# Kernel tuning notes

Measured on AMD Instinct MI355X. Metric: run time of the kernel, lower is better.

Reference implementation:

```python
import jax, jax.numpy as jnp
import numpy as np

EMBED = 1024
HEADS = 16
HEAD_DIM = EMBED // HEADS


def setup_inputs() -> dict:
    key = jax.random.key(0)
    k1, k2, k3, k4, k5, k6 = jax.random.split(key, 6)
    N, S = 4, 2048
    return {
        "values": jax.random.normal(k1, (N, S, EMBED), dtype=jnp.float32),
        "keys": jax.random.normal(k2, (N, S, EMBED), dtype=jnp.float32),
        "query": jax.random.normal(k3, (N, S, EMBED), dtype=jnp.float32),
        "mask": jax.random.randint(k4, (N, 1, S, S), 0, 2, dtype=jnp.int32),
        "W_out": jax.random.normal(k5, (EMBED, EMBED), dtype=jnp.float32) * (1.0 / np.sqrt(EMBED)),
        "b_out": jax.random.normal(k6, (EMBED,), dtype=jnp.float32) * 0.01,
    }


def reference(values, keys, query, mask, W_out, b_out):
    N, Q = query.shape[0], query.shape[1]
    K = keys.shape[1]
    v = values.reshape(N, K, HEADS, HEAD_DIM)
    k = keys.reshape(N, K, HEADS, HEAD_DIM)
    q = query.reshape(N, Q, HEADS, HEAD_DIM)
    # [N,H,Q,K] score matrix (materialized, as in the original)
    energy = jnp.einsum("nqhd,nkhd->nhqk", q, k)
    energy = jnp.where(mask == 0, jnp.float32(-1e20), energy)
    # NOTE: original scales by sqrt(embed_size), not sqrt(head_dim)
    attn = jax.nn.softmax(energy / jnp.sqrt(jnp.float32(EMBED)), axis=3)
    out = jnp.einsum("nhqk,nkhd->nqhd", attn, v).reshape(N, Q, EMBED)
    return out @ W_out.T + b_out
```

## Files before the change

kernel.cpp:

```cpp
#include <hip/hip_runtime.h>
#include <stdint.h>

#define SEQ 2048
#define NB 4
#define NHD 16
#define HD 64
#define EMB 1024

typedef unsigned short u16;
typedef unsigned int u32;
typedef unsigned long long u64;
typedef __bf16 bf16x8 __attribute__((ext_vector_type(8)));
typedef float f32x4 __attribute__((ext_vector_type(4)));

__device__ __forceinline__ u16 f2bf(float f) {
    u32 u = __builtin_bit_cast(u32, f);
    u32 r = u + 0x7FFFu + ((u >> 16) & 1u);
    return (u16)(r >> 16);
}

__device__ __forceinline__ float exp2_hw(float x) {
    float r;
    asm("v_exp_f32 %0, %1" : "=v"(r) : "v"(x));
    return r;
}

__device__ __forceinline__ u32 cvtpk_bf16(float lo, float hi) {
    u32 r;
    asm("v_cvt_pk_bf16_f32 %0, %1, %2" : "=v"(r) : "v"(lo), "v"(hi));
    return r;
}

__device__ __forceinline__ void gld16(const void* g, void* l) {
    __builtin_amdgcn_global_load_lds(
        (const __attribute__((address_space(1))) u32*)g,
        (__attribute__((address_space(3))) u32*)l, 16, 0, 0);
}

__global__ void prep_qk(const float* __restrict__ q, const float* __restrict__ k,
                        u16* __restrict__ qb, u16* __restrict__ kb) {
    int tid = blockIdx.x * 256 + threadIdx.x;
    int unit = tid >> 4;
    int dq = (tid & 15) << 2;
    int h = unit & (NHD - 1);
    int ns = unit >> 4;
    int n = ns >> 11, s = ns & (SEQ - 1);
    size_t src = (size_t)ns * EMB + h * HD + dq;
    float4 qv = *(const float4*)(q + src);
    float4 kv = *(const float4*)(k + src);
    size_t dst = ((size_t)(n * NHD + h) * SEQ + s) * HD + dq;
    const float QS = 0.04508422f;
    ushort4 qo, ko;
    qo.x = f2bf(qv.x * QS); qo.y = f2bf(qv.y * QS);
    qo.z = f2bf(qv.z * QS); qo.w = f2bf(qv.w * QS);
    ko.x = f2bf(kv.x); ko.y = f2bf(kv.y); ko.z = f2bf(kv.z); ko.w = f2bf(kv.w);
    *(ushort4*)(qb + dst) = qo;
    *(ushort4*)(kb + dst) = ko;
}

__global__ void prep_v(const float* __restrict__ v, u16* __restrict__ vt) {
    __shared__ float t[64][65];
    int s0 = blockIdx.x << 6, h = blockIdx.y, n = blockIdx.z;
    int tid = threadIdx.x;
    int c = (tid & 15) << 2;
    int r0 = tid >> 4;
#pragma unroll
    for (int it = 0; it < 4; it++) {
        int r = r0 + (it << 4);
        float4 val = *(const float4*)(v + ((size_t)n * SEQ + s0 + r) * EMB + h * HD + c);
        t[c][r] = val.x; t[c + 1][r] = val.y; t[c + 2][r] = val.z; t[c + 3][r] = val.w;
    }
    __syncthreads();
    int d = tid >> 2, so = (tid & 3) << 4;
    size_t dst = ((size_t)(n * NHD + h) * HD + d) * SEQ + s0 + so;
#pragma unroll
    for (int j = 0; j < 4; j++) {
        ushort4 o;
        o.x = f2bf(t[d][so + 4 * j + 0]); o.y = f2bf(t[d][so + 4 * j + 1]);
        o.z = f2bf(t[d][so + 4 * j + 2]); o.w = f2bf(t[d][so + 4 * j + 3]);
        *(ushort4*)(vt + dst + 4 * j) = o;
    }
}

__global__ void prep_w(const float* __restrict__ w, u16* __restrict__ wb) {
    int tid = blockIdx.x * 256 + threadIdx.x;
    float4 v = *(const float4*)(w + (size_t)tid * 4);
    ushort4 o;
    o.x = f2bf(v.x); o.y = f2bf(v.y); o.z = f2bf(v.z); o.w = f2bf(v.w);
    *(ushort4*)(wb + (size_t)tid * 4) = o;
}

__global__ __launch_bounds__(256, 4) void attn_k(
    const u16* __restrict__ qb, const u16* __restrict__ kb,
    const u16* __restrict__ vt, const int* __restrict__ mask,
    u16* __restrict__ ao)
{
    __shared__ __align__(16) u16 lds_k[2][64 * 64];
    __shared__ __align__(16) u16 lds_v[2][64 * 64];
    __shared__ __align__(16) u16 lds_p[4][16 * 64];
    const int tid = threadIdx.x;
    const int wave = tid >> 6, lane = tid & 63;
    const int g = lane >> 4, c16 = lane & 15;
    const int bid = blockIdx.x;
    const int swz = (bid & 7) * 256 + (bid >> 3);
    const int n = swz >> 9, h = (swz >> 5) & 15, qt = swz & 31;
    const int qw = (qt << 6) + (wave << 4);
    const size_t nh = (size_t)(n * NHD + h);
    const u16* Qp = qb + nh * SEQ * HD;
    const u16* Kp = kb + nh * SEQ * HD;
    const u16* Vp = vt + nh * HD * SEQ;
    const int* mrow = mask + ((size_t)n * SEQ + qw + c16) * SEQ;

    bf16x8 qa0 = *(const bf16x8*)(Qp + (size_t)(qw + c16) * HD + 8 * g);
    bf16x8 qa1 = *(const bf16x8*)(Qp + (size_t)(qw + c16) * HD + 8 * g + 32);

    f32x4 o[4];
#pragma unroll
    for (int i = 0; i < 4; i++) o[i] = (f32x4){0.f, 0.f, 0.f, 0.f};
    float m_r = -INFINITY, l_r = 0.f;

    auto STAGE = [&](int buf, int kt) {
        int k0 = kt << 6;
#pragma unroll
        for (int i = 0; i < 2; i++) {
            int off = (i << 8) + tid;
            int row = off >> 3;
            int sch = (off & 7) ^ (row & 7);
            int ldso = ((i << 8) + (wave << 6)) << 3;
            gld16(Kp + (size_t)(k0 + row) * HD + (sch << 3), &lds_k[buf][ldso]);
            gld16(Vp + (size_t)row * SEQ + k0 + (sch << 3), &lds_v[buf][ldso]);
        }
    };

    auto COMPUTE = [&](int buf, int kt) {
        f32x4 s[4];
#pragma unroll
        for (int t = 0; t < 4; t++) {
            int4 mv = *(const int4*)(mrow + (kt << 6) + (t << 4) + (g << 2));
            s[t][0] = fmaf((float)mv.x, 1e20f, -1e20f);
            s[t][1] = fmaf((float)mv.y, 1e20f, -1e20f);
            s[t][2] = fmaf((float)mv.z, 1e20f, -1e20f);
            s[t][3] = fmaf((float)mv.w, 1e20f, -1e20f);
        }
#pragma unroll
        for (int t = 0; t < 4; t++) {
            int kc = (t << 4) + c16;
            int sw = (kc & 7) << 3;
            bf16x8 kf0 = *(const bf16x8*)&lds_k[buf][kc * 64 + ((8 * g) ^ sw)];
            bf16x8 kf1 = *(const bf16x8*)&lds_k[buf][kc * 64 + ((8 * g + 32) ^ sw)];
            s[t] = __builtin_amdgcn_mfma_f32_16x16x32_bf16(kf0, qa0, s[t], 0, 0, 0);
            s[t] = __builtin_amdgcn_mfma_f32_16x16x32_bf16(kf1, qa1, s[t], 0, 0, 0);
        }
        float pmax = fmaxf(fmaxf(fmaxf(s[0][0], s[0][1]), fmaxf(s[0][2], s[0][3])),
                           fmaxf(fmaxf(s[1][0], s[1][1]), fmaxf(s[1][2], s[1][3])));
        pmax = fmaxf(pmax, fmaxf(fmaxf(fmaxf(s[2][0], s[2][1]), fmaxf(s[2][2], s[2][3])),
                                 fmaxf(fmaxf(s[3][0], s[3][1]), fmaxf(s[3][2], s[3][3]))));
        pmax = fmaxf(pmax, __shfl_xor(pmax, 16));
        pmax = fmaxf(pmax, __shfl_xor(pmax, 32));
        if (__ballot(pmax > m_r + 8.f)) {
            float mnew = fmaxf(m_r, pmax);
            float sc = exp2_hw(m_r - mnew);
            m_r = mnew;
            l_r *= sc;
#pragma unroll
            for (int dt = 0; dt < 4; dt++) o[dt] *= sc;
        }
        float ladd = 0.f;
        u32 pk[4][2];
#pragma unroll
        for (int t = 0; t < 4; t++) {
            float p0 = exp2_hw(s[t][0] - m_r);
            float p1 = exp2_hw(s[t][1] - m_r);
            float p2 = exp2_hw(s[t][2] - m_r);
            float p3 = exp2_hw(s[t][3] - m_r);
            ladd += (p0 + p1) + (p2 + p3);
            pk[t][0] = cvtpk_bf16(p0, p1);
            pk[t][1] = cvtpk_bf16(p2, p3);
        }
        ladd += __shfl_xor(ladd, 16);
        ladd += __shfl_xor(ladd, 32);
        l_r += ladd;
        char* pbase = (char*)&lds_p[wave][0];
        int swp = (c16 & 7) << 4;
#pragma unroll
        for (int t = 0; t < 4; t++) {
            u64 w2 = ((u64)pk[t][1] << 32) | pk[t][0];
            *(u64*)(pbase + ((c16 * 128 + 32 * t + 8 * g) ^ swp)) = w2;
        }
        bf16x8 pa0 = *(const bf16x8*)(pbase + ((c16 * 128 + 16 * g) ^ swp));
        bf16x8 pa1 = *(const bf16x8*)(pbase + ((c16 * 128 + 64 + 16 * g) ^ swp));
#pragma unroll
        for (int dt = 0; dt < 4; dt++) {
            int dr = (dt << 4) + c16;
            int swv = (dr & 7) << 3;
            bf16x8 vf0 = *(const bf16x8*)&lds_v[buf][dr * 64 + ((8 * g) ^ swv)];
            bf16x8 vf1 = *(const bf16x8*)&lds_v[buf][dr * 64 + ((8 * g + 32) ^ swv)];
            o[dt] = __builtin_amdgcn_mfma_f32_16x16x32_bf16(vf0, pa0, o[dt], 0, 0, 0);
            o[dt] = __builtin_amdgcn_mfma_f32_16x16x32_bf16(vf1, pa1, o[dt], 0, 0, 0);
        }
    };

    STAGE(0, 0);
    __syncthreads();
    for (int kt = 0; kt < SEQ / 64; kt++) {
        int buf = kt & 1;
        if (kt + 1 < SEQ / 64) STAGE(buf ^ 1, kt + 1);
        COMPUTE(buf, kt);
        __syncthreads();
    }

    float inv = 1.f / l_r;
    size_t obase = ((size_t)n * SEQ + qw + c16) * EMB + h * HD;
#pragma unroll
    for (int dt = 0; dt < 4; dt++) {
        u32 w0 = cvtpk_bf16(o[dt][0] * inv, o[dt][1] * inv);
        u32 w1 = cvtpk_bf16(o[dt][2] * inv, o[dt][3] * inv);
        u64 w2 = ((u64)w1 << 32) | w0;
        *(u64*)(ao + obase + (dt << 4) + (g << 2)) = w2;
    }
}

__global__ __launch_bounds__(256, 2) void proj_k(
    const u16* __restrict__ a, const u16* __restrict__ w,
    const float* __restrict__ bias, float* __restrict__ out)
{
    __shared__ __align__(16) u16 lds_a[2][128 * 64];
    __shared__ __align__(16) u16 lds_b[2][128 * 64];
    const int tid = threadIdx.x;
    const int wave = tid >> 6, lane = tid & 63;
    const int g = lane >> 4, c16 = lane & 15;
    const int m0 = blockIdx.y << 7, n0 = blockIdx.x << 7;
    const int wm = wave >> 1, wn = wave & 1;
    f32x4 acc[4][4];
#pragma unroll
    for (int i = 0; i < 4; i++)
#pragma unroll
        for (int j = 0; j < 4; j++) acc[i][j] = (f32x4){0.f, 0.f, 0.f, 0.f};

    auto STAGE = [&](int buf, int k0) {
#pragma unroll
        for (int i = 0; i < 4; i++) {
            int off = (i << 8) + tid;
            int row = off >> 3;
            int sch = (off & 7) ^ (row & 7);
            int ldso = ((i << 8) + (wave << 6)) << 3;
            gld16(a + (size_t)(m0 + row) * EMB + k0 + (sch << 3), &lds_a[buf][ldso]);
            gld16(w + (size_t)(n0 + row) * EMB + k0 + (sch << 3), &lds_b[buf][ldso]);
        }
    };

    auto COMP = [&](int buf) {
#pragma unroll
        for (int c = 0; c < 2; c++) {
            bf16x8 af[4], bfr[4];
#pragma unroll
            for (int mt = 0; mt < 4; mt++) {
                int row = (wm << 6) + (mt << 4) + c16;
                af[mt] = *(const bf16x8*)&lds_a[buf][row * 64 + ((8 * g + 32 * c) ^ ((row & 7) << 3))];
            }
#pragma unroll
            for (int nt = 0; nt < 4; nt++) {
                int row = (wn << 6) + (nt << 4) + c16;
                bfr[nt] = *(const bf16x8*)&lds_b[buf][row * 64 + ((8 * g + 32 * c) ^ ((row & 7) << 3))];
            }
#pragma unroll
            for (int mt = 0; mt < 4; mt++)
#pragma unroll
                for (int nt = 0; nt < 4; nt++)
                    acc[mt][nt] = __builtin_amdgcn_mfma_f32_16x16x32_bf16(af[mt], bfr[nt], acc[mt][nt], 0, 0, 0);
        }
    };

    STAGE(0, 0);
    __syncthreads();
    for (int ki = 0; ki < EMB / 64; ki++) {
        int buf = ki & 1;
        if (ki + 1 < EMB / 64) STAGE(buf ^ 1, (ki + 1) << 6);
        COMP(buf);
        __syncthreads();
    }

#pragma unroll
    for (int nt = 0; nt < 4; nt++) {
        int col = n0 + (wn << 6) + (nt << 4) + c16;
        float bv = bias[col];
#pragma unroll
        for (int mt = 0; mt < 4; mt++) {
#pragma unroll
            for (int r = 0; r < 4; r++) {
                int row = m0 + (wm << 6) + (mt << 4) + 4 * g + r;
                out[(size_t)row * EMB + col] = acc[mt][nt][r] + bv;
            }
        }
    }
}

extern "C" void kernel_launch(void* const* d_in, const int* in_sizes, int n_in,
                              void* d_out, int out_size, void* d_ws, size_t ws_size,
                              hipStream_t stream) {
    const float* V = (const float*)d_in[0];
    const float* K = (const float*)d_in[1];
    const float* Q = (const float*)d_in[2];
    const int* M = (const int*)d_in[3];
    const float* W = (const float*)d_in[4];
    const float* B = (const float*)d_in[5];
    float* out = (float*)d_out;

    char* ws = (char*)d_ws;
    u16* qb = (u16*)(ws);
    u16* kb = (u16*)(ws + ((size_t)16 << 20));
    u16* vt = (u16*)(ws + ((size_t)32 << 20));
    u16* wb = (u16*)(ws + ((size_t)48 << 20));
    u16* ao = (u16*)(ws + ((size_t)50 << 20));

    prep_qk<<<8192, 256, 0, stream>>>(Q, K, qb, kb);
    prep_v<<<dim3(SEQ / 64, NHD, NB), 256, 0, stream>>>(V, vt);
    prep_w<<<1024, 256, 0, stream>>>(W, wb);
    attn_k<<<2048, 256, 0, stream>>>(qb, kb, vt, M, ao);
    proj_k<<<dim3(EMB / 128, (NB * SEQ) / 128), 256, 0, stream>>>(ao, wb, B, out);
}
```

Before: 397.3 us.

## Pack attention mask into bitmasks before the attention kernel

Adds a preprocessing kernel that converts the int32 mask into 64-bit ballot bitmasks, permuted to match the MFMA lane layout. The attention kernel then loads one u64 per key tile instead of four int4 loads per lane. This cuts the mask bytes the attention kernel reads for every head by about 32x. The cost is an extra kernel pass over the full mask and 2 MB of workspace.

```diff
diff --git a/kernel.cpp b/kernel.cpp
--- a/kernel.cpp
+++ b/kernel.cpp
@@ -82,6 +82,18 @@
     }
 }
 
+__global__ void prep_mask(const int* __restrict__ m, u64* __restrict__ mb) {
+    int gw = (blockIdx.x * 256 + threadIdx.x) >> 6;
+    int lane = threadIdx.x & 63;
+    int src = ((lane & 12) << 2) | ((lane & 48) >> 2) | (lane & 3);
+    for (int i = 0; i < 64; i++) {
+        size_t widx = (size_t)gw * 64 + i;
+        int v = m[widx * 64 + src];
+        u64 b = __ballot(v != 0);
+        if (lane == 0) mb[widx] = b;
+    }
+}
+
 __global__ void prep_w(const float* __restrict__ w, u16* __restrict__ wb) {
     int tid = blockIdx.x * 256 + threadIdx.x;
     float4 v = *(const float4*)(w + (size_t)tid * 4);
@@ -92,7 +104,7 @@
 
 __global__ __launch_bounds__(256, 4) void attn_k(
     const u16* __restrict__ qb, const u16* __restrict__ kb,
-    const u16* __restrict__ vt, const int* __restrict__ mask,
+    const u16* __restrict__ vt, const u64* __restrict__ mbits,
     u16* __restrict__ ao)
 {
     __shared__ __align__(16) u16 lds_k[2][64 * 64];
@@ -109,7 +121,7 @@
     const u16* Qp = qb + nh * SEQ * HD;
     const u16* Kp = kb + nh * SEQ * HD;
     const u16* Vp = vt + nh * HD * SEQ;
-    const int* mrow = mask + ((size_t)n * SEQ + qw + c16) * SEQ;
+    const u64* mrow = mbits + ((size_t)n * SEQ + qw + c16) * (SEQ / 64);
 
     bf16x8 qa0 = *(const bf16x8*)(Qp + (size_t)(qw + c16) * HD + 8 * g);
     bf16x8 qa1 = *(const bf16x8*)(Qp + (size_t)(qw + c16) * HD + 8 * g + 32);
@@ -133,15 +145,14 @@
     };
 
     auto COMPUTE = [&](int buf, int kt) {
+        u64 mw_cur = mrow[kt];
+        u32 mloc = (u32)(mw_cur >> (g << 4)) & 0xFFFFu;
         f32x4 s[4];
 #pragma unroll
-        for (int t = 0; t < 4; t++) {
-            int4 mv = *(const int4*)(mrow + (kt << 6) + (t << 4) + (g << 2));
-            s[t][0] = fmaf((float)mv.x, 1e20f, -1e20f);
-            s[t][1] = fmaf((float)mv.y, 1e20f, -1e20f);
-            s[t][2] = fmaf((float)mv.z, 1e20f, -1e20f);
-            s[t][3] = fmaf((float)mv.w, 1e20f, -1e20f);
-        }
+        for (int t = 0; t < 4; t++)
+#pragma unroll
+            for (int r = 0; r < 4; r++)
+                s[t][r] = ((mloc >> ((t << 2) | r)) & 1u) ? 0.f : -1e20f;
 #pragma unroll
         for (int t = 0; t < 4; t++) {
             int kc = (t << 4) + c16;
@@ -310,12 +321,14 @@
     u16* qb = (u16*)(ws);
     u16* kb = (u16*)(ws + ((size_t)16 << 20));
     u16* vt = (u16*)(ws + ((size_t)32 << 20));
-    u16* wb = (u16*)(ws + ((size_t)48 << 20));
-    u16* ao = (u16*)(ws + ((size_t)50 << 20));
+    u64* mb = (u64*)(ws + ((size_t)48 << 20));
+    u16* wb = (u16*)(ws + ((size_t)50 << 20));
+    u16* ao = (u16*)(ws + ((size_t)52 << 20));
 
     prep_qk<<<8192, 256, 0, stream>>>(Q, K, qb, kb);
     prep_v<<<dim3(SEQ / 64, NHD, NB), 256, 0, stream>>>(V, vt);
+    prep_mask<<<1024, 256, 0, stream>>>(M, mb);
     prep_w<<<1024, 256, 0, stream>>>(W, wb);
-    attn_k<<<2048, 256, 0, stream>>>(qb, kb, vt, M, ao);
+    attn_k<<<2048, 256, 0, stream>>>(qb, kb, vt, mb, ao);
     proj_k<<<dim3(EMB / 128, (NB * SEQ) / 128), 256, 0, stream>>>(ao, wb, B, out);
 }
```

After: 376.7 us. 1.05x faster.
